# Optimization experiments

Measured on AMD Instinct MI355X. Metric: run time of the kernel, lower is better.

## Reference

```python
import jax, jax.numpy as jnp
import numpy as np

B, T, D, H = 4, 2048, 1024, 16
DH = D // H

def setup_inputs() -> dict:
    key = jax.random.key(0)
    k1, k2, k3 = jax.random.split(key, 3)
    x = jax.random.normal(k1, (B, T, D), dtype=jnp.float32)
    w_qkv = jax.random.normal(k2, (D, 3 * D), dtype=jnp.float32) * (1.0 / np.sqrt(D))
    w_out = jax.random.normal(k3, (D, D), dtype=jnp.float32) * (1.0 / np.sqrt(D))
    return {"x": x, "w_qkv": w_qkv, "w_out": w_out}

def reference(x, w_qkv, w_out):
    Bq, Tq, C = x.shape
    qkv = x @ w_qkv                                   # [B,T,3D]
    q, k, v = jnp.split(qkv, 3, axis=-1)
    q = q.reshape(Bq, Tq, H, DH).transpose(0, 2, 1, 3)  # [B,H,T,dh]
    k = k.reshape(Bq, Tq, H, DH).transpose(0, 2, 1, 3)
    v = v.reshape(Bq, Tq, H, DH).transpose(0, 2, 1, 3)
    scores = jnp.einsum('bhqd,bhkd->bhqk', q, k) / jnp.sqrt(jnp.float32(DH))
    mask = jnp.tril(jnp.ones((Tq, Tq), dtype=bool))
    scores = jnp.where(mask, scores, jnp.float32(-jnp.inf))
    attn = jax.nn.softmax(scores, axis=-1)
    out = jnp.einsum('bhqk,bhkd->bhqd', attn, v)      # [B,H,T,dh]
    out = out.transpose(0, 2, 1, 3).reshape(Bq, Tq, C)
    return out @ w_out
```

## Files before the change

kernel.cpp:

```cpp
#include <hip/hip_runtime.h>

#define B_ 4
#define T_ 2048
#define D_ 1024
#define H_ 16
#define DH_ 64
#define BH_ (B_*H_)
#define M_ (B_*T_)
#define N3_ (3*D_)

typedef __attribute__((ext_vector_type(8))) __bf16 bf16x8;
typedef __attribute__((ext_vector_type(4))) float f32x4;
typedef __attribute__((ext_vector_type(16))) float f32x16;
typedef __attribute__((ext_vector_type(8))) unsigned short u16x8;
typedef __attribute__((ext_vector_type(4))) unsigned short u16x4;
typedef int i32x2 __attribute__((ext_vector_type(2)));

__device__ inline void gload_lds16(const void* g, void* l) {
  __builtin_amdgcn_global_load_lds((const __attribute__((address_space(1))) void*)g,
                                   (__attribute__((address_space(3))) void*)l, 16, 0, 0);
}

__device__ inline unsigned short f2bf(float v) {
  __bf16 t = (__bf16)v;
  return *(unsigned short*)&t;
}

__device__ inline float bf2f(unsigned short u) {
  unsigned x = ((unsigned)u) << 16;
  return __builtin_bit_cast(float, x);
}

__device__ inline unsigned pk2(float lo, float hi2) {
  return (unsigned)f2bf(lo) | ((unsigned)f2bf(hi2) << 16);
}

template<int BASE>
__device__ inline bf16x8 buildP(const f32x16& S) {
  unsigned a = pk2(S[BASE+0], S[BASE+1]);
  unsigned b = pk2(S[BASE+2], S[BASE+3]);
  unsigned c = pk2(S[BASE+4], S[BASE+5]);
  unsigned d = pk2(S[BASE+6], S[BASE+7]);
  i32x2 r0 = __builtin_amdgcn_permlane32_swap((int)a, (int)c, false, false);
  i32x2 r1 = __builtin_amdgcn_permlane32_swap((int)b, (int)d, false, false);
  union { unsigned u[4]; bf16x8 v; } U;
  U.u[0] = (unsigned)r0[0];
  U.u[1] = (unsigned)r1[0];
  U.u[2] = (unsigned)r0[1];
  U.u[3] = (unsigned)r1[1];
  return U.v;
}

__global__ void prep(const float* __restrict__ x, unsigned short* __restrict__ xb,
                     const float* __restrict__ wq, unsigned short* __restrict__ wqT,
                     const float* __restrict__ wo, unsigned short* __restrict__ woT) {
  __shared__ unsigned short lds[64][72];
  int bid = blockIdx.x, tid = threadIdx.x;
  if (bid < 4096) {
    int i = bid * 256 + tid;
    const float4* p = (const float4*)(x + (size_t)i * 8);
    float4 a = p[0], b = p[1];
    float v[8] = {a.x, a.y, a.z, a.w, b.x, b.y, b.z, b.w};
    u16x8 r;
#pragma unroll
    for (int j = 0; j < 8; ++j) r[j] = f2bf(v[j]);
    *(u16x8*)(xb + (size_t)i * 8) = r;
    return;
  }
  const float* w;
  unsigned short* wt;
  int n0, k0, Ndim;
  if (bid < 4096 + 768) {
    int b2 = bid - 4096;
    w = wq; wt = wqT; Ndim = N3_;
    n0 = (b2 % 48) * 64; k0 = (b2 / 48) * 64;
  } else {
    int b3 = bid - 4864;
    w = wo; wt = woT; Ndim = D_;
    n0 = (b3 % 16) * 64; k0 = (b3 / 16) * 64;
  }
#pragma unroll
  for (int i = 0; i < 2; ++i) {
    int idx = i * 256 + tid;
    int r = idx >> 3, c8 = idx & 7;
    const float4* src = (const float4*)(w + (size_t)(k0 + r) * Ndim + n0 + c8 * 8);
    float4 a = src[0], b = src[1];
    float v[8] = {a.x, a.y, a.z, a.w, b.x, b.y, b.z, b.w};
#pragma unroll
    for (int j = 0; j < 8; ++j) lds[r][c8 * 8 + j] = f2bf(v[j]);
  }
  __syncthreads();
#pragma unroll
  for (int i = 0; i < 2; ++i) {
    int idx = i * 256 + tid;
    int r = idx >> 3, c8 = idx & 7;
    u16x8 o;
#pragma unroll
    for (int j = 0; j < 8; ++j) o[j] = lds[c8 * 8 + j][r];
    *(u16x8*)(wt + (size_t)(n0 + r) * 1024 + k0 + c8 * 8) = o;
  }
}

__global__ __launch_bounds__(256) void gemm2b(
    const unsigned short* __restrict__ A,
    const unsigned short* __restrict__ BT,
    int epi,
    unsigned short* __restrict__ qb, unsigned short* __restrict__ kb, unsigned short* __restrict__ vtb,
    float* __restrict__ outf) {
  extern __shared__ __align__(16) char lds[];
  const int tid = threadIdx.x;
  const int wave = tid >> 6, lane = tid & 63, g = lane >> 4, c = lane & 15;
  const int wm = wave >> 1, wn = wave & 1;
  int flat = blockIdx.y * gridDim.x + blockIdx.x;
  int xcd = flat & 7, local = flat >> 3;
  int bx = xcd * 8 + (local & 7);
  int by = local >> 3;
  const int m0 = bx * 128, n0 = by * 128;

  f32x4 acc[4][4] = {};

  auto stage = [&](int slot, int jj) {
    char* sb = lds + slot * 32768;
#pragma unroll
    for (int i = 0; i < 4; ++i) {
      int idx = i * 256 + tid;
      int r = idx >> 3, s = idx & 7;
      gload_lds16(A + (size_t)(m0 + r) * 1024 + jj * 64 + 8 * (s ^ (r & 7)),
                  sb + idx * 16);
    }
#pragma unroll
    for (int i = 0; i < 4; ++i) {
      int idx = i * 256 + tid;
      int r = idx >> 3, s = idx & 7;
      gload_lds16(BT + (size_t)(n0 + r) * 1024 + jj * 64 + 8 * (s ^ (r & 7)),
                  sb + 16384 + idx * 16);
    }
  };

  stage(0, 0);
  for (int j = 0; j < 16; ++j) {
    if (j < 15) {
      stage((j + 1) & 1, j + 1);
      asm volatile("s_waitcnt vmcnt(8)" ::: "memory");
    } else {
      asm volatile("s_waitcnt vmcnt(0)" ::: "memory");
    }
    __builtin_amdgcn_s_barrier();
    asm volatile("" ::: "memory");

    const char* sA = lds + (j & 1) * 32768;
    const char* sB = sA + 16384;
#pragma unroll
    for (int kc = 0; kc < 2; ++kc) {
      bf16x8 af[4], bf[4];
#pragma unroll
      for (int mt = 0; mt < 4; ++mt) {
        int r = wm * 64 + mt * 16 + c;
        af[mt] = *(const bf16x8*)(sA + r * 128 + 16 * ((kc * 4 + g) ^ (r & 7)));
      }
#pragma unroll
      for (int nt = 0; nt < 4; ++nt) {
        int r = wn * 64 + nt * 16 + c;
        bf[nt] = *(const bf16x8*)(sB + r * 128 + 16 * ((kc * 4 + g) ^ (r & 7)));
      }
      __builtin_amdgcn_s_setprio(1);
#pragma unroll
      for (int mt = 0; mt < 4; ++mt)
#pragma unroll
        for (int nt = 0; nt < 4; ++nt)
          acc[mt][nt] = __builtin_amdgcn_mfma_f32_16x16x32_bf16(af[mt], bf[nt], acc[mt][nt], 0, 0, 0);
      __builtin_amdgcn_s_setprio(0);
    }

    __builtin_amdgcn_s_barrier();
    asm volatile("" ::: "memory");
  }

  if (epi == 0) {
    int which = n0 >> 10;
    int colbase = n0 - (which << 10);
    if (which == 2) {
#pragma unroll
      for (int mt = 0; mt < 4; ++mt)
#pragma unroll
        for (int nt = 0; nt < 4; ++nt) {
          int m = m0 + wm * 64 + mt * 16 + g * 4;
          int n = colbase + wn * 64 + nt * 16 + c;
          int b = m >> 11, t = m & 2047;
          int h = n >> 6, d = n & 63;
          u16x4 pk;
#pragma unroll
          for (int i = 0; i < 4; ++i) pk[i] = f2bf(acc[mt][nt][i]);
          *(u16x4*)(vtb + ((size_t)(b * H_ + h) * 64 + d) * T_ + t) = pk;
        }
    } else {
      unsigned short* dst = which == 0 ? qb : kb;
      float scale = which == 0 ? 0.18033688011112042f : 1.0f;
#pragma unroll
      for (int mt = 0; mt < 4; ++mt)
#pragma unroll
        for (int nt = 0; nt < 4; ++nt)
#pragma unroll
          for (int i = 0; i < 4; ++i) {
            int m = m0 + wm * 64 + mt * 16 + g * 4 + i;
            int n = colbase + wn * 64 + nt * 16 + c;
            int b = m >> 11, t = m & 2047;
            int h = n >> 6, d = n & 63;
            dst[(((size_t)(b * H_ + h) * T_ + t) << 6) + d] = f2bf(acc[mt][nt][i] * scale);
          }
    }
  } else {
#pragma unroll
    for (int mt = 0; mt < 4; ++mt)
#pragma unroll
      for (int nt = 0; nt < 4; ++nt)
#pragma unroll
        for (int i = 0; i < 4; ++i) {
          int m = m0 + wm * 64 + mt * 16 + g * 4 + i;
          int n = n0 + wn * 64 + nt * 16 + c;
          outf[(size_t)m * 1024 + n] = acc[mt][nt][i];
        }
  }
}

#define PV_STEP(PF, KC)                                                                \
  {                                                                                    \
    bf16x8 pf = (PF);                                                                  \
    int dr0 = q32, dr1 = 32 + q32;                                                     \
    bf16x8 v0 = *(const bf16x8*)(sV + dr0 * 128 + 16 * (((KC)*2 + hi) ^ (dr0 & 7)));   \
    bf16x8 v1 = *(const bf16x8*)(sV + dr1 * 128 + 16 * (((KC)*2 + hi) ^ (dr1 & 7)));   \
    oT0 = __builtin_amdgcn_mfma_f32_32x32x16_bf16(v0, pf, oT0, 0, 0, 0);               \
    oT1 = __builtin_amdgcn_mfma_f32_32x32x16_bf16(v1, pf, oT1, 0, 0, 0);               \
  }

__global__ __launch_bounds__(512) void attn(
    const unsigned short* __restrict__ qbp,
    const unsigned short* __restrict__ kb,
    const unsigned short* __restrict__ vt,
    unsigned short* __restrict__ ao,
    unsigned short* __restrict__ opart,
    float* __restrict__ lpart) {
  __shared__ __align__(16) char pool[49152];
  const int tid = threadIdx.x;
  const int wave = tid >> 6, lane = tid & 63;
  const int q32 = lane & 31, hi = lane >> 5;
  const int bh = blockIdx.y;

  int u;
  switch (blockIdx.x) {
    case 0: u = 5; break; case 1: u = 4; break; case 2: u = 3; break;
    case 3: u = 8; break; case 4: u = 9; break; case 5: u = 6; break;
    case 6: u = 7; break; case 7: u = 2; break; case 8: u = 1; break;
    default: u = 0; break;
  }
  int pb, k0t, nt, pidx;
  bool part;
  if (u < 6)      { pb = u; k0t = 0;            nt = 4 * u + 4; part = false; pidx = 0; }
  else if (u < 8) { pb = 6; k0t = 14 * (u - 6); nt = 14; part = true; pidx = (bh * 2 + 0) * 2 + (u - 6); }
  else            { pb = 7; k0t = 16 * (u - 8); nt = 16; part = true; pidx = (bh * 2 + 1) * 2 + (u - 8); }
  const int k1t = k0t + nt - 1;
  const int q0w = pb * 256 + wave * 32;
  const int dtile = 4 * pb + (wave >> 1);

  bf16x8 qf[4];
#pragma unroll
  for (int dhc = 0; dhc < 4; ++dhc)
    qf[dhc] = *(const bf16x8*)(qbp + ((size_t)bh * T_ + q0w + q32) * 64 + dhc * 16 + hi * 8);

  f32x16 oT0 = {}, oT1 = {};
  float l_run = 0.0f;

  auto stage = [&](int buf, int kt) {
    int r = tid >> 3, s8 = tid & 7;
    gload_lds16(kb + ((size_t)bh * T_ + kt * 64 + r) * 64 + 8 * (s8 ^ (r & 7)),
                pool + buf * 16384 + tid * 16);
    gload_lds16(vt + ((size_t)bh * 64 + r) * T_ + kt * 64 + 8 * (s8 ^ (r & 7)),
                pool + buf * 16384 + 8192 + tid * 16);
  };

  stage(0, k0t);
  stage(1, k0t + 1);
  int sj = 0;
  for (int kt = k0t; kt <= k1t; ++kt) {
    asm volatile("s_waitcnt vmcnt(2)" ::: "memory");
    __builtin_amdgcn_s_barrier();
    asm volatile("" ::: "memory");
    int st2 = sj + 2; if (st2 >= 3) st2 -= 3;
    if (kt + 2 <= k1t) stage(st2, kt + 2);
    if (kt <= dtile) {
      const char* sK = pool + sj * 16384;
      const char* sV = sK + 8192;

      f32x16 st0 = {}, st1 = {};
      __builtin_amdgcn_s_setprio(1);
#pragma unroll
      for (int dhc = 0; dhc < 4; ++dhc) {
        int kr0 = q32, kr1 = 32 + q32;
        bf16x8 k0 = *(const bf16x8*)(sK + kr0 * 128 + 16 * ((dhc * 2 + hi) ^ (kr0 & 7)));
        bf16x8 k1 = *(const bf16x8*)(sK + kr1 * 128 + 16 * ((dhc * 2 + hi) ^ (kr1 & 7)));
        st0 = __builtin_amdgcn_mfma_f32_32x32x16_bf16(k0, qf[dhc], st0, 0, 0, 0);
        st1 = __builtin_amdgcn_mfma_f32_32x32x16_bf16(k1, qf[dhc], st1, 0, 0, 0);
      }
      __builtin_amdgcn_s_setprio(0);

      if (kt == dtile) {
        int qg = q0w + q32;
#pragma unroll
        for (int r = 0; r < 16; ++r) {
          int krow = kt * 64 + (r & 3) + 8 * (r >> 2) + 4 * hi;
          if (krow > qg) st0[r] = -INFINITY;
          if (krow + 32 > qg) st1[r] = -INFINITY;
        }
      }

      float ps0 = 0.0f, ps1 = 0.0f, ps2 = 0.0f, ps3 = 0.0f;
#pragma unroll
      for (int r = 0; r < 16; r += 4) {
        float a0 = __builtin_amdgcn_exp2f(st0[r + 0]); st0[r + 0] = a0; ps0 += a0;
        float a1 = __builtin_amdgcn_exp2f(st0[r + 1]); st0[r + 1] = a1; ps1 += a1;
        float a2 = __builtin_amdgcn_exp2f(st0[r + 2]); st0[r + 2] = a2; ps2 += a2;
        float a3 = __builtin_amdgcn_exp2f(st0[r + 3]); st0[r + 3] = a3; ps3 += a3;
      }
#pragma unroll
      for (int r = 0; r < 16; r += 4) {
        float a0 = __builtin_amdgcn_exp2f(st1[r + 0]); st1[r + 0] = a0; ps0 += a0;
        float a1 = __builtin_amdgcn_exp2f(st1[r + 1]); st1[r + 1] = a1; ps1 += a1;
        float a2 = __builtin_amdgcn_exp2f(st1[r + 2]); st1[r + 2] = a2; ps2 += a2;
        float a3 = __builtin_amdgcn_exp2f(st1[r + 3]); st1[r + 3] = a3; ps3 += a3;
      }
      float ps = (ps0 + ps1) + (ps2 + ps3);
      ps += __shfl_xor(ps, 32);
      l_run += ps;

      __builtin_amdgcn_s_setprio(1);
      PV_STEP(buildP<0>(st0), 0)
      PV_STEP(buildP<8>(st0), 1)
      PV_STEP(buildP<0>(st1), 2)
      PV_STEP(buildP<8>(st1), 3)
      __builtin_amdgcn_s_setprio(0);
    }
    sj = sj + 1; if (sj >= 3) sj -= 3;
  }

  __syncthreads();
  unsigned short* ep = (unsigned short*)pool + wave * (32 * 72);
  float inv_l = part ? 1.0f : (1.0f / l_run);
  if (part && hi == 0) lpart[pidx * 256 + wave * 32 + q32] = l_run;
#pragma unroll
  for (int r = 0; r < 16; ++r) {
    int d0 = (r & 3) + 8 * (r >> 2) + 4 * hi;
    ep[q32 * 72 + d0]      = f2bf(oT0[r] * inv_l);
    ep[q32 * 72 + 32 + d0] = f2bf(oT1[r] * inv_l);
  }
  __syncthreads();
  {
    int q = lane >> 1, half = lane & 1;
    const unsigned short* row = ep + q * 72 + half * 32;
    unsigned short* g;
    if (part) {
      g = opart + ((size_t)pidx * 256 + wave * 32 + q) * 64 + half * 32;
    } else {
      int t = q0w + q;
      int b = bh >> 4, h = bh & 15;
      g = ao + ((size_t)(b * T_ + t)) * 1024 + h * 64 + half * 32;
    }
#pragma unroll
    for (int j = 0; j < 4; ++j)
      *(u16x8*)(g + j * 8) = *(const u16x8*)(row + j * 8);
  }
}

__global__ __launch_bounds__(256) void combine(
    const unsigned short* __restrict__ opart, const float* __restrict__ lpart,
    unsigned short* __restrict__ ao) {
  int pair = blockIdx.x;
  int bh = pair >> 1, pb = 6 + (pair & 1);
  int tid = threadIdx.x;
  int rloc = tid >> 2, dc = tid & 3;
  const unsigned short* A = opart + ((size_t)(pair * 2 + 0)) * 256 * 64;
  const unsigned short* Bp = opart + ((size_t)(pair * 2 + 1)) * 256 * 64;
  const float* lA = lpart + (pair * 2 + 0) * 256;
  const float* lB = lpart + (pair * 2 + 1) * 256;
  int b = bh >> 4, hh = bh & 15;
#pragma unroll
  for (int rr = 0; rr < 4; ++rr) {
    int row = rr * 64 + rloc;
    float inv = 1.0f / (lA[row] + lB[row]);
    const unsigned short* pa = A + row * 64 + dc * 16;
    const unsigned short* pbp = Bp + row * 64 + dc * 16;
    u16x8 a0 = *(const u16x8*)pa, a1 = *(const u16x8*)(pa + 8);
    u16x8 b0 = *(const u16x8*)pbp, b1 = *(const u16x8*)(pbp + 8);
    u16x8 o0, o1;
#pragma unroll
    for (int j = 0; j < 8; ++j) {
      o0[j] = f2bf((bf2f(a0[j]) + bf2f(b0[j])) * inv);
      o1[j] = f2bf((bf2f(a1[j]) + bf2f(b1[j])) * inv);
    }
    int t = pb * 256 + row;
    unsigned short* g = ao + ((size_t)(b * T_ + t)) * 1024 + hh * 64 + dc * 16;
    *(u16x8*)g = o0;
    *(u16x8*)(g + 8) = o1;
  }
}

extern "C" void kernel_launch(void* const* d_in, const int* in_sizes, int n_in,
                              void* d_out, int out_size, void* d_ws, size_t ws_size,
                              hipStream_t stream) {
  const float* x = (const float*)d_in[0];
  const float* w_qkv = (const float*)d_in[1];
  const float* w_out = (const float*)d_in[2];
  float* out = (float*)d_out;

  char* ws = (char*)d_ws;
  size_t off = 0;
  auto alloc = [&](size_t bytes) {
    char* p = ws + off;
    off += (bytes + 255) & ~(size_t)255;
    return p;
  };
  unsigned short* xb    = (unsigned short*)alloc((size_t)M_ * D_ * 2);
  unsigned short* wqkvT = (unsigned short*)alloc((size_t)N3_ * D_ * 2);
  unsigned short* woutT = (unsigned short*)alloc((size_t)D_ * D_ * 2);
  unsigned short* qbuf  = (unsigned short*)alloc((size_t)BH_ * T_ * 64 * 2);
  unsigned short* kbuf  = (unsigned short*)alloc((size_t)BH_ * T_ * 64 * 2);
  unsigned short* vtb   = (unsigned short*)alloc((size_t)BH_ * 64 * T_ * 2);
  unsigned short* opart = (unsigned short*)alloc((size_t)256 * 256 * 64 * 2);
  float*          lpart = (float*)alloc((size_t)256 * 256 * 4);
  unsigned short* ao    = xb;

  hipFuncSetAttribute(reinterpret_cast<const void*>(gemm2b),
                      hipFuncAttributeMaxDynamicSharedMemorySize, 65536);

  prep<<<4096 + 768 + 256, 256, 0, stream>>>(x, xb, w_qkv, wqkvT, w_out, woutT);
  gemm2b<<<dim3(M_ / 128, N3_ / 128), 256, 65536, stream>>>(xb, wqkvT, 0, qbuf, kbuf, vtb, nullptr);
  attn<<<dim3(10, BH_), 512, 0, stream>>>(qbuf, kbuf, vtb, ao, opart, lpart);
  combine<<<128, 256, 0, stream>>>(opart, lpart, ao);
  gemm2b<<<dim3(M_ / 128, D_ / 128), 256, 65536, stream>>>(ao, woutT, 1, nullptr, nullptr, nullptr, out);
}
```

Before: 164.7 us.

## Balance causal attention work by pairing long and short query strips per block

Each attention block now handles two query strips (7-h and h) and splits each strip's key range in two halves by blockIdx.y parity. This gives every block the same number of key tiles, replacing the earlier 10-way hand-tuned schedule. All strips now write unnormalized partials, and the combine kernel merges partials for all 512 strips, which adds partial write and read traffic. The main GEMM k-loop is also fully unrolled.

After: 151.7 us. 1.09x faster.

```diff
diff --git a/kernel.cpp b/kernel.cpp
--- a/kernel.cpp
+++ b/kernel.cpp
@@ -138,6 +138,7 @@
   };
 
   stage(0, 0);
+#pragma unroll
   for (int j = 0; j < 16; ++j) {
     if (j < 15) {
       stage((j + 1) & 1, j + 1);
@@ -237,38 +238,15 @@
     const unsigned short* __restrict__ qbp,
     const unsigned short* __restrict__ kb,
     const unsigned short* __restrict__ vt,
-    unsigned short* __restrict__ ao,
     unsigned short* __restrict__ opart,
     float* __restrict__ lpart) {
   __shared__ __align__(16) char pool[49152];
   const int tid = threadIdx.x;
   const int wave = tid >> 6, lane = tid & 63;
   const int q32 = lane & 31, hi = lane >> 5;
-  const int bh = blockIdx.y;
-
-  int u;
-  switch (blockIdx.x) {
-    case 0: u = 5; break; case 1: u = 4; break; case 2: u = 3; break;
-    case 3: u = 8; break; case 4: u = 9; break; case 5: u = 6; break;
-    case 6: u = 7; break; case 7: u = 2; break; case 8: u = 1; break;
-    default: u = 0; break;
-  }
-  int pb, k0t, nt, pidx;
-  bool part;
-  if (u < 6)      { pb = u; k0t = 0;            nt = 4 * u + 4; part = false; pidx = 0; }
-  else if (u < 8) { pb = 6; k0t = 14 * (u - 6); nt = 14; part = true; pidx = (bh * 2 + 0) * 2 + (u - 6); }
-  else            { pb = 7; k0t = 16 * (u - 8); nt = 16; part = true; pidx = (bh * 2 + 1) * 2 + (u - 8); }
-  const int k1t = k0t + nt - 1;
-  const int q0w = pb * 256 + wave * 32;
-  const int dtile = 4 * pb + (wave >> 1);
-
-  bf16x8 qf[4];
-#pragma unroll
-  for (int dhc = 0; dhc < 4; ++dhc)
-    qf[dhc] = *(const bf16x8*)(qbp + ((size_t)bh * T_ + q0w + q32) * 64 + dhc * 16 + hi * 8);
-
-  f32x16 oT0 = {}, oT1 = {};
-  float l_run = 0.0f;
+  const int bh = blockIdx.x;
+  const int y = blockIdx.y;
+  const int h = y >> 1, odd = y & 1;
 
   auto stage = [&](int buf, int kt) {
     int r = tid >> 3, s8 = tid & 7;
@@ -278,95 +256,107 @@
                 pool + buf * 16384 + 8192 + tid * 16);
   };
 
-  stage(0, k0t);
-  stage(1, k0t + 1);
-  int sj = 0;
-  for (int kt = k0t; kt <= k1t; ++kt) {
-    asm volatile("s_waitcnt vmcnt(2)" ::: "memory");
-    __builtin_amdgcn_s_barrier();
-    asm volatile("" ::: "memory");
-    int st2 = sj + 2; if (st2 >= 3) st2 -= 3;
-    if (kt + 2 <= k1t) stage(st2, kt + 2);
-    if (kt <= dtile) {
-      const char* sK = pool + sj * 16384;
-      const char* sV = sK + 8192;
-
-      f32x16 st0 = {}, st1 = {};
-      __builtin_amdgcn_s_setprio(1);
-#pragma unroll
-      for (int dhc = 0; dhc < 4; ++dhc) {
-        int kr0 = q32, kr1 = 32 + q32;
-        bf16x8 k0 = *(const bf16x8*)(sK + kr0 * 128 + 16 * ((dhc * 2 + hi) ^ (kr0 & 7)));
-        bf16x8 k1 = *(const bf16x8*)(sK + kr1 * 128 + 16 * ((dhc * 2 + hi) ^ (kr1 & 7)));
-        st0 = __builtin_amdgcn_mfma_f32_32x32x16_bf16(k0, qf[dhc], st0, 0, 0, 0);
-        st1 = __builtin_amdgcn_mfma_f32_32x32x16_bf16(k1, qf[dhc], st1, 0, 0, 0);
+#pragma unroll
+  for (int seg = 0; seg < 2; ++seg) {
+    const int pb  = seg == 0 ? 7 - h : h;
+    const int len = seg == 0 ? 16 - 2 * h : 2 * h + 2;
+    const int k0t = odd * len;
+    const int k1t = k0t + len - 1;
+    const int pidx = (bh * 8 + pb) * 2 + odd;
+    const int q0w = pb * 256 + wave * 32;
+    const int dtile = 4 * pb + (wave >> 1);
+
+    bf16x8 qf[4];
+#pragma unroll
+    for (int dhc = 0; dhc < 4; ++dhc)
+      qf[dhc] = *(const bf16x8*)(qbp + ((size_t)bh * T_ + q0w + q32) * 64 + dhc * 16 + hi * 8);
+
+    f32x16 oT0 = {}, oT1 = {};
+    float l_run = 0.0f;
+
+    stage(0, k0t);
+    stage(1, k0t + 1);
+    int sj = 0;
+    for (int kt = k0t; kt <= k1t; ++kt) {
+      asm volatile("s_waitcnt vmcnt(2)" ::: "memory");
+      __builtin_amdgcn_s_barrier();
+      asm volatile("" ::: "memory");
+      int st2 = sj + 2; if (st2 >= 3) st2 -= 3;
+      if (kt + 2 <= k1t) stage(st2, kt + 2);
+      if (kt <= dtile) {
+        const char* sK = pool + sj * 16384;
+        const char* sV = sK + 8192;
+
+        f32x16 st0 = {}, st1 = {};
+        __builtin_amdgcn_s_setprio(1);
+#pragma unroll
+        for (int dhc = 0; dhc < 4; ++dhc) {
+          int kr0 = q32, kr1 = 32 + q32;
+          bf16x8 k0 = *(const bf16x8*)(sK + kr0 * 128 + 16 * ((dhc * 2 + hi) ^ (kr0 & 7)));
+          bf16x8 k1 = *(const bf16x8*)(sK + kr1 * 128 + 16 * ((dhc * 2 + hi) ^ (kr1 & 7)));
+          st0 = __builtin_amdgcn_mfma_f32_32x32x16_bf16(k0, qf[dhc], st0, 0, 0, 0);
+          st1 = __builtin_amdgcn_mfma_f32_32x32x16_bf16(k1, qf[dhc], st1, 0, 0, 0);
+        }
+        __builtin_amdgcn_s_setprio(0);
+
+        if (kt == dtile) {
+          int qg = q0w + q32;
+#pragma unroll
+          for (int r = 0; r < 16; ++r) {
+            int krow = kt * 64 + (r & 3) + 8 * (r >> 2) + 4 * hi;
+            if (krow > qg) st0[r] = -INFINITY;
+            if (krow + 32 > qg) st1[r] = -INFINITY;
+          }
+        }
+
+        float ps0 = 0.0f, ps1 = 0.0f, ps2 = 0.0f, ps3 = 0.0f;
+#pragma unroll
+        for (int r = 0; r < 16; r += 4) {
+          float a0 = __builtin_amdgcn_exp2f(st0[r + 0]); st0[r + 0] = a0; ps0 += a0;
+          float a1 = __builtin_amdgcn_exp2f(st0[r + 1]); st0[r + 1] = a1; ps1 += a1;
+          float a2 = __builtin_amdgcn_exp2f(st0[r + 2]); st0[r + 2] = a2; ps2 += a2;
+          float a3 = __builtin_amdgcn_exp2f(st0[r + 3]); st0[r + 3] = a3; ps3 += a3;
+        }
+#pragma unroll
+        for (int r = 0; r < 16; r += 4) {
+          float a0 = __builtin_amdgcn_exp2f(st1[r + 0]); st1[r + 0] = a0; ps0 += a0;
+          float a1 = __builtin_amdgcn_exp2f(st1[r + 1]); st1[r + 1] = a1; ps1 += a1;
+          float a2 = __builtin_amdgcn_exp2f(st1[r + 2]); st1[r + 2] = a2; ps2 += a2;
+          float a3 = __builtin_amdgcn_exp2f(st1[r + 3]); st1[r + 3] = a3; ps3 += a3;
+        }
+        float ps = (ps0 + ps1) + (ps2 + ps3);
+        ps += __shfl_xor(ps, 32);
+        l_run += ps;
+
+        __builtin_amdgcn_s_setprio(1);
+        PV_STEP(buildP<0>(st0), 0)
+        PV_STEP(buildP<8>(st0), 1)
+        PV_STEP(buildP<0>(st1), 2)
+        PV_STEP(buildP<8>(st1), 3)
+        __builtin_amdgcn_s_setprio(0);
       }
-      __builtin_amdgcn_s_setprio(0);
-
-      if (kt == dtile) {
-        int qg = q0w + q32;
-#pragma unroll
-        for (int r = 0; r < 16; ++r) {
-          int krow = kt * 64 + (r & 3) + 8 * (r >> 2) + 4 * hi;
-          if (krow > qg) st0[r] = -INFINITY;
-          if (krow + 32 > qg) st1[r] = -INFINITY;
-        }
-      }
-
-      float ps0 = 0.0f, ps1 = 0.0f, ps2 = 0.0f, ps3 = 0.0f;
-#pragma unroll
-      for (int r = 0; r < 16; r += 4) {
-        float a0 = __builtin_amdgcn_exp2f(st0[r + 0]); st0[r + 0] = a0; ps0 += a0;
-        float a1 = __builtin_amdgcn_exp2f(st0[r + 1]); st0[r + 1] = a1; ps1 += a1;
-        float a2 = __builtin_amdgcn_exp2f(st0[r + 2]); st0[r + 2] = a2; ps2 += a2;
-        float a3 = __builtin_amdgcn_exp2f(st0[r + 3]); st0[r + 3] = a3; ps3 += a3;
-      }
-#pragma unroll
-      for (int r = 0; r < 16; r += 4) {
-        float a0 = __builtin_amdgcn_exp2f(st1[r + 0]); st1[r + 0] = a0; ps0 += a0;
-        float a1 = __builtin_amdgcn_exp2f(st1[r + 1]); st1[r + 1] = a1; ps1 += a1;
-        float a2 = __builtin_amdgcn_exp2f(st1[r + 2]); st1[r + 2] = a2; ps2 += a2;
-        float a3 = __builtin_amdgcn_exp2f(st1[r + 3]); st1[r + 3] = a3; ps3 += a3;
-      }
-      float ps = (ps0 + ps1) + (ps2 + ps3);
-      ps += __shfl_xor(ps, 32);
-      l_run += ps;
-
-      __builtin_amdgcn_s_setprio(1);
-      PV_STEP(buildP<0>(st0), 0)
-      PV_STEP(buildP<8>(st0), 1)
-      PV_STEP(buildP<0>(st1), 2)
-      PV_STEP(buildP<8>(st1), 3)
-      __builtin_amdgcn_s_setprio(0);
-    }
-    sj = sj + 1; if (sj >= 3) sj -= 3;
-  }
-
-  __syncthreads();
-  unsigned short* ep = (unsigned short*)pool + wave * (32 * 72);
-  float inv_l = part ? 1.0f : (1.0f / l_run);
-  if (part && hi == 0) lpart[pidx * 256 + wave * 32 + q32] = l_run;
-#pragma unroll
-  for (int r = 0; r < 16; ++r) {
-    int d0 = (r & 3) + 8 * (r >> 2) + 4 * hi;
-    ep[q32 * 72 + d0]      = f2bf(oT0[r] * inv_l);
-    ep[q32 * 72 + 32 + d0] = f2bf(oT1[r] * inv_l);
-  }
-  __syncthreads();
-  {
-    int q = lane >> 1, half = lane & 1;
-    const unsigned short* row = ep + q * 72 + half * 32;
-    unsigned short* g;
-    if (part) {
-      g = opart + ((size_t)pidx * 256 + wave * 32 + q) * 64 + half * 32;
-    } else {
-      int t = q0w + q;
-      int b = bh >> 4, h = bh & 15;
-      g = ao + ((size_t)(b * T_ + t)) * 1024 + h * 64 + half * 32;
-    }
-#pragma unroll
-    for (int j = 0; j < 4; ++j)
-      *(u16x8*)(g + j * 8) = *(const u16x8*)(row + j * 8);
+      sj = sj + 1; if (sj >= 3) sj -= 3;
+    }
+
+    __syncthreads();
+    if (hi == 0) lpart[pidx * 256 + wave * 32 + q32] = l_run;
+    unsigned short* ep = (unsigned short*)pool + wave * (32 * 72);
+#pragma unroll
+    for (int r = 0; r < 16; ++r) {
+      int d0 = (r & 3) + 8 * (r >> 2) + 4 * hi;
+      ep[q32 * 72 + d0]      = f2bf(oT0[r]);
+      ep[q32 * 72 + 32 + d0] = f2bf(oT1[r]);
+    }
+    __syncthreads();
+    {
+      int q = lane >> 1, half = lane & 1;
+      const unsigned short* row = ep + q * 72 + half * 32;
+      unsigned short* g = opart + ((size_t)pidx * 256 + wave * 32 + q) * 64 + half * 32;
+#pragma unroll
+      for (int j = 0; j < 4; ++j)
+        *(u16x8*)(g + j * 8) = *(const u16x8*)(row + j * 8);
+    }
+    if (seg == 0) __syncthreads();
   }
 }
 
@@ -374,10 +364,10 @@
     const unsigned short* __restrict__ opart, const float* __restrict__ lpart,
     unsigned short* __restrict__ ao) {
   int pair = blockIdx.x;
-  int bh = pair >> 1, pb = 6 + (pair & 1);
+  int bh = pair >> 3, strip = pair & 7;
   int tid = threadIdx.x;
   int rloc = tid >> 2, dc = tid & 3;
-  const unsigned short* A = opart + ((size_t)(pair * 2 + 0)) * 256 * 64;
+  const unsigned short* A  = opart + ((size_t)(pair * 2 + 0)) * 256 * 64;
   const unsigned short* Bp = opart + ((size_t)(pair * 2 + 1)) * 256 * 64;
   const float* lA = lpart + (pair * 2 + 0) * 256;
   const float* lB = lpart + (pair * 2 + 1) * 256;
@@ -386,9 +376,9 @@
   for (int rr = 0; rr < 4; ++rr) {
     int row = rr * 64 + rloc;
     float inv = 1.0f / (lA[row] + lB[row]);
-    const unsigned short* pa = A + row * 64 + dc * 16;
+    const unsigned short* pa  = A + row * 64 + dc * 16;
     const unsigned short* pbp = Bp + row * 64 + dc * 16;
-    u16x8 a0 = *(const u16x8*)pa, a1 = *(const u16x8*)(pa + 8);
+    u16x8 a0 = *(const u16x8*)pa,  a1 = *(const u16x8*)(pa + 8);
     u16x8 b0 = *(const u16x8*)pbp, b1 = *(const u16x8*)(pbp + 8);
     u16x8 o0, o1;
 #pragma unroll
@@ -396,7 +386,7 @@
       o0[j] = f2bf((bf2f(a0[j]) + bf2f(b0[j])) * inv);
       o1[j] = f2bf((bf2f(a1[j]) + bf2f(b1[j])) * inv);
     }
-    int t = pb * 256 + row;
+    int t = strip * 256 + row;
     unsigned short* g = ao + ((size_t)(b * T_ + t)) * 1024 + hh * 64 + dc * 16;
     *(u16x8*)g = o0;
     *(u16x8*)(g + 8) = o1;
@@ -424,8 +414,8 @@
   unsigned short* qbuf  = (unsigned short*)alloc((size_t)BH_ * T_ * 64 * 2);
   unsigned short* kbuf  = (unsigned short*)alloc((size_t)BH_ * T_ * 64 * 2);
   unsigned short* vtb   = (unsigned short*)alloc((size_t)BH_ * 64 * T_ * 2);
-  unsigned short* opart = (unsigned short*)alloc((size_t)256 * 256 * 64 * 2);
-  float*          lpart = (float*)alloc((size_t)256 * 256 * 4);
+  unsigned short* opart = (unsigned short*)alloc((size_t)BH_ * 8 * 2 * 256 * 64 * 2);
+  float*          lpart = (float*)alloc((size_t)BH_ * 8 * 2 * 256 * 4);
   unsigned short* ao    = xb;
 
   hipFuncSetAttribute(reinterpret_cast<const void*>(gemm2b),
@@ -433,7 +423,7 @@
 
   prep<<<4096 + 768 + 256, 256, 0, stream>>>(x, xb, w_qkv, wqkvT, w_out, woutT);
   gemm2b<<<dim3(M_ / 128, N3_ / 128), 256, 65536, stream>>>(xb, wqkvT, 0, qbuf, kbuf, vtb, nullptr);
-  attn<<<dim3(10, BH_), 512, 0, stream>>>(qbuf, kbuf, vtb, ao, opart, lpart);
-  combine<<<128, 256, 0, stream>>>(opart, lpart, ao);
+  attn<<<dim3(BH_, 8), 512, 0, stream>>>(qbuf, kbuf, vtb, opart, lpart);
+  combine<<<BH_ * 8, 256, 0, stream>>>(opart, lpart, ao);
   gemm2b<<<dim3(M_ / 128, D_ / 128), 256, 65536, stream>>>(ao, woutT, 1, nullptr, nullptr, nullptr, out);
 }
```
